# Kernel optimization log

Hardware: AMD Instinct MI355X
Metric: run time of the kernel (lower is better)

## Reference

```python
import jax, jax.numpy as jnp
import numpy as np

IMG = 32            # feature-map side == image_size
B, HC = 8, 3        # batch, hint channels
C, NH, L = 256, 8, 8  # model_channels, nhead, num_encoder_layers
DFF = 1025
HIN = IMG * 8       # hint resolution (three stride-2 convs => /8)
NEIGH = (7, 7)
CONV_SHAPES = [(16, HC), (16, 16), (32, 16), (32, 32), (96, 32), (96, 96), (256, 96), (C, 256)]
STRIDES = [1, 1, 2, 1, 2, 1, 2, 1]


def setup_inputs() -> dict:
    key = jax.random.key(0)
    ks = jax.random.split(key, 32)
    inp = {"hint": jax.random.normal(ks[0], (B, HC, HIN, HIN), jnp.float32)}
    for i, (co, ci) in enumerate(CONV_SHAPES):
        inp[f"conv_w{i}"] = jax.random.normal(ks[1 + i], (co, ci, 3, 3), jnp.float32) * 0.05
    base = 9
    def p(shape, j):
        return jax.random.normal(ks[base + j], (L,) + shape, jnp.float32) * 0.02
    inp["in_proj_w"] = p((3 * C, C), 0)
    inp["in_proj_b"] = p((3 * C,), 1)
    inp["out_w"] = p((C, C), 2)
    inp["out_b"] = p((C,), 3)
    inp["lin1_w"] = p((DFF, C), 4)
    inp["lin1_b"] = p((DFF,), 5)
    inp["lin2_w"] = p((C, DFF), 6)
    inp["lin2_b"] = p((C,), 7)
    inp["ln1_w"] = jnp.ones((L, C), jnp.float32)
    inp["ln1_b"] = jnp.zeros((L, C), jnp.float32)
    inp["ln2_w"] = jnp.ones((L, C), jnp.float32)
    inp["ln2_b"] = jnp.zeros((L, C), jnp.float32)
    return inp


def _conv(x, w, s):
    # torch Conv2d(k=3, padding=1, stride=s, bias=False)
    return jax.lax.conv_general_dilated(x, w, (s, s), [(1, 1), (1, 1)],
                                        dimension_numbers=("NCHW", "OIHW", "NCHW"))


def _sine_pos(h, w, c):
    # DETR/UniAD PositionEmbeddingSine (normalize=False, temperature=1e4) -> (h*w, c)
    npf = c // 2
    y = jnp.broadcast_to(jnp.arange(1, h + 1, dtype=jnp.float32)[:, None], (h, w))
    x = jnp.broadcast_to(jnp.arange(1, w + 1, dtype=jnp.float32)[None, :], (h, w))
    dim_t = 10000.0 ** (2.0 * (jnp.arange(npf, dtype=jnp.float32) // 2) / npf)
    px = x[..., None] / dim_t
    py = y[..., None] / dim_t
    px = jnp.stack([jnp.sin(px[..., 0::2]), jnp.cos(px[..., 1::2])], -1).reshape(h, w, npf)
    py = jnp.stack([jnp.sin(py[..., 0::2]), jnp.cos(py[..., 1::2])], -1).reshape(h, w, npf)
    return jnp.concatenate([py, px], -1).reshape(h * w, c)


def _neigh_mask(h, w, hm, wm):
    # vectorized version of generate_mask: 0 inside the hm x wm neighborhood, -inf outside
    ih = jnp.arange(h)
    iw = jnp.arange(w)
    dh = jnp.abs(ih[:, None] - ih[None, :]) <= hm // 2   # (h, h)
    dw = jnp.abs(iw[:, None] - iw[None, :]) <= wm // 2   # (w, w)
    allowed = (dh[:, None, :, None] & dw[None, :, None, :]).reshape(h * w, h * w)
    return jnp.where(allowed, 0.0, -1e9).astype(jnp.float32)


def _ln(x, g, b):
    mu = x.mean(-1, keepdims=True)
    v = ((x - mu) ** 2).mean(-1, keepdims=True)
    return (x - mu) / jnp.sqrt(v + 1e-5) * g + b


def _forward(hint, conv_ws, params):
    x = hint
    for i, (w, s) in enumerate(zip(conv_ws, STRIDES)):
        x = _conv(x, w, s)
        if i < len(conv_ws) - 1:
            x = jax.nn.silu(x)
    b, c, h, w = x.shape
    src = x.reshape(b, c, h * w).transpose(0, 2, 1)          # (B, N, C), N h-major
    pos = _sine_pos(h, w, c)[None]                           # (1, N, C)
    mask = _neigh_mask(h, w, *NEIGH)                         # (N, N)
    dh = c // NH
    scale = 1.0 / np.sqrt(dh).astype(np.float32)

    def layer(s, p):
        ipw, ipb, ow, ob, l1w, l1b, l2w, l2b, g1, b1, g2, b2 = p
        qk_in = s + pos
        q = (qk_in @ ipw[:c].T + ipb[:c]).reshape(b, -1, NH, dh)
        k = (qk_in @ ipw[c:2 * c].T + ipb[c:2 * c]).reshape(b, -1, NH, dh)
        v = (s @ ipw[2 * c:].T + ipb[2 * c:]).reshape(b, -1, NH, dh)
        sc = jnp.einsum('bnhd,bmhd->bhnm', q, k) * scale + mask
        a = jax.nn.softmax(sc, -1)
        ctx = jnp.einsum('bhnm,bmhd->bnhd', a, v).reshape(b, -1, c)
        s = _ln(s + ctx @ ow.T + ob, g1, b1)                 # post-norm
        ff = jax.nn.relu(s @ l1w.T + l1b) @ l2w.T + l2b      # dropout inactive (eval)
        return _ln(s + ff, g2, b2), None

    src, _ = jax.lax.scan(layer, src, params)
    return src.transpose(0, 2, 1).reshape(b, c, h, w)        # '(h w) b c -> b c h w'


def reference(hint, conv_w0, conv_w1, conv_w2, conv_w3, conv_w4, conv_w5, conv_w6, conv_w7,
              in_proj_w, in_proj_b, out_w, out_b, lin1_w, lin1_b, lin2_w, lin2_b,
              ln1_w, ln1_b, ln2_w, ln2_b):
    conv_ws = (conv_w0, conv_w1, conv_w2, conv_w3, conv_w4, conv_w5, conv_w6, conv_w7)
    params = (in_proj_w, in_proj_b, out_w, out_b, lin1_w, lin1_b, lin2_w, lin2_b,
              ln1_w, ln1_b, ln2_w, ln2_b)
    return _forward(hint, conv_ws, params)
```

## Files before the change

### kernel.cpp

```cpp
#include <hip/hip_runtime.h>
#include <hip/hip_bf16.h>


typedef __bf16 bf16x8 __attribute__((ext_vector_type(8)));
typedef float f32x4 __attribute__((ext_vector_type(4)));
typedef unsigned short us8v __attribute__((ext_vector_type(8)));

__device__ __forceinline__ unsigned short f2bf(float f) {
  unsigned int u = __float_as_uint(f);
  unsigned int r = (u + 0x7fffu + ((u >> 16) & 1u)) >> 16;
  return (unsigned short)r;
}
__device__ __forceinline__ float bf2f(unsigned short h) {
  return __uint_as_float(((unsigned int)h) << 16);
}

#define GLD16(src, dst)                                                        \
  __builtin_amdgcn_global_load_lds(                                            \
      (const __attribute__((address_space(1))) unsigned int*)(src),            \
      (__attribute__((address_space(3))) unsigned int*)(dst), 16, 0, 0)

template<int BM, int BN, int NT, int MODE, int LNF = 0, int KTC = 0>
__global__ __launch_bounds__(NT) void k_gemm(
    const unsigned short* __restrict__ A, int lda,
    const unsigned short* __restrict__ Bw, int ldb,
    const float* __restrict__ bias, const float* __restrict__ posadd,
    float* __restrict__ C, unsigned short* __restrict__ Cb, int ldc,
    int K, int Nstore, int act, int omode, long long zsB, long long zsC,
    const unsigned short* __restrict__ zpage, int Ci, int Hi, int stride, int lw,
    int divm, int divs, const float* __restrict__ lng, const float* __restrict__ lnb)
{
  constexpr int NW = NT / 64;
  constexpr int NWN = (NT == 512) ? 4 : ((BN >= 128) ? 2 : 1);
  constexpr int NWM = NW / NWN;
  constexpr int WM = BM / NWM, WN = BN / NWN;
  constexpr int MF = WM / 16, NF = WN / 16;
  constexpr int AIS = (BM * 8) / NT;
  constexpr int BIS = (BN * 8) / NT;
  __shared__ unsigned short lA[2][BM * 64];
  __shared__ unsigned short lB[2][BN * 64];
  int tid = threadIdx.x, lane = tid & 63, wid = tid >> 6;
  int bm = blockIdx.x * BM, bn = blockIdx.y * BN;
  const unsigned short* Bz = Bw + (size_t)blockIdx.z * zsB;

  int j = (lane & 7) ^ (lane >> 3);
  int e8 = (j & 3) << 3;
  int halfl = j >> 2;

  size_t arow[AIS], brow[BIS];
  int hb[AIS], wb[AIS];
  size_t ab[AIS];
#pragma unroll
  for (int i = 0; i < AIS; ++i) {
    int rr = (wid + i * NW) * 8 + (lane >> 3);
    if constexpr (MODE == 0) {
      arow[i] = (size_t)(bm + rr) * lda + (j << 3);
    } else {
      int pos = bm + rr;
      int b = pos >> (2 * lw);
      int rem = pos & ((1 << (2 * lw)) - 1);
      int ho = rem >> lw, wo = rem & ((1 << lw) - 1);
      hb[i] = ho * stride - 1;
      wb[i] = wo * stride - 1;
      ab[i] = (size_t)b * Hi * Hi * Ci;
    }
  }
#pragma unroll
  for (int i = 0; i < BIS; ++i)
    brow[i] = (size_t)(bn + (wid + i * NW) * 8 + (lane >> 3)) * ldb + (j << 3);

  auto stage = [&](int buf, int kt) {
    if constexpr (MODE == 1) {
      int s0 = kt * 2, s1 = s0 + 1;
      int t0 = (s0 * divm) >> divs, t1 = (s1 * divm) >> divs;
      int cipw = Ci >> 5;
      int cc0 = (s0 - t0 * cipw) << 5, cc1 = (s1 - t1 * cipw) << 5;
      int kh0 = (t0 * 171) >> 9, kw0 = t0 - kh0 * 3;
      int kh1 = (t1 * 171) >> 9, kw1 = t1 - kh1 * 3;
      int kh = halfl ? kh1 : kh0;
      int kw = halfl ? kw1 : kw0;
      int cco = halfl ? cc1 : cc0;
      bool tv = (halfl ? t1 : t0) < 9;
#pragma unroll
      for (int i = 0; i < AIS; ++i) {
        int hi = hb[i] + kh, wi = wb[i] + kw;
        const unsigned short* ap =
            (tv && (unsigned)hi < (unsigned)Hi && (unsigned)wi < (unsigned)Hi)
                ? (A + ab[i] + (size_t)(hi * Hi + wi) * Ci + cco + e8)
                : zpage;
        GLD16(ap, &lA[buf][(wid + i * NW) * 512]);
      }
    } else {
#pragma unroll
      for (int i = 0; i < AIS; ++i)
        GLD16(A + arow[i] + kt * 64, &lA[buf][(wid + i * NW) * 512]);
    }
#pragma unroll
    for (int i = 0; i < BIS; ++i)
      GLD16(Bz + brow[i] + kt * 64, &lB[buf][(wid + i * NW) * 512]);
  };

  f32x4 acc[MF][NF];
#pragma unroll
  for (int m = 0; m < MF; ++m)
#pragma unroll
    for (int n = 0; n < NF; ++n)
#pragma unroll
      for (int q = 0; q < 4; ++q) acc[m][n][q] = 0.f;

  int wn = wid % NWN, wm = wid / NWN;
  int r0 = wm * WM + (lane & 15);
  int c0 = wn * WN + (lane & 15);
  int sl0 = (((lane >> 4)) ^ (lane & 7)) << 3;
  int sl1 = (((lane >> 4) + 4) ^ (lane & 7)) << 3;
  const int nkt = (KTC > 0) ? KTC : (K >> 6);
  int cur = 0;
  stage(0, 0);
#pragma unroll
  for (int kt = 0; kt < nkt; ++kt) {
    if (kt + 1 < nkt) {
      stage(cur ^ 1, kt + 1);
      asm volatile("s_waitcnt vmcnt(%0)" : : "n"(AIS + BIS) : "memory");
    } else {
      asm volatile("s_waitcnt vmcnt(0)" : : : "memory");
    }
    __builtin_amdgcn_s_barrier();
    asm volatile("" ::: "memory");
    bf16x8 a0[MF], a1[MF], b0[NF], b1[NF];
#pragma unroll
    for (int m = 0; m < MF; ++m) {
      a0[m] = *(const bf16x8*)&lA[cur][(r0 + m * 16) * 64 + sl0];
      a1[m] = *(const bf16x8*)&lA[cur][(r0 + m * 16) * 64 + sl1];
    }
#pragma unroll
    for (int n = 0; n < NF; ++n) {
      b0[n] = *(const bf16x8*)&lB[cur][(c0 + n * 16) * 64 + sl0];
      b1[n] = *(const bf16x8*)&lB[cur][(c0 + n * 16) * 64 + sl1];
    }
#pragma unroll
    for (int m = 0; m < MF; ++m)
#pragma unroll
      for (int n = 0; n < NF; ++n)
        acc[m][n] = __builtin_amdgcn_mfma_f32_16x16x32_bf16(a0[m], b0[n], acc[m][n], 0, 0, 0);
#pragma unroll
    for (int m = 0; m < MF; ++m)
#pragma unroll
      for (int n = 0; n < NF; ++n)
        acc[m][n] = __builtin_amdgcn_mfma_f32_16x16x32_bf16(a1[m], b1[n], acc[m][n], 0, 0, 0);
    asm volatile("" ::: "memory");
    __builtin_amdgcn_s_barrier();
    cur ^= 1;
  }

  int colb = bn + wn * WN + (lane & 15);
  int rowb = bm + wm * WM + ((lane >> 4) << 2);
  float* Cz = C ? C + (size_t)blockIdx.z * zsC : nullptr;
  unsigned short* Cbz = Cb ? Cb + (size_t)blockIdx.z * zsC : nullptr;
#pragma unroll
  for (int n = 0; n < NF; ++n) {
    int col = colb + n * 16;
    if (col >= Nstore) continue;
    float bs = bias ? bias[col] : 0.f;
#pragma unroll
    for (int m = 0; m < MF; ++m) {
#pragma unroll
      for (int q = 0; q < 4; ++q) {
        int row = rowb + m * 16 + q;
        float v = acc[m][n][q] + bs;
        if (posadd && col < 512) v += posadd[((row & 1023) << 9) + col];
        if (act == 1) v = fmaxf(v, 0.f);
        else if (act == 2) v = v / (1.f + __expf(-v));
        size_t off = (size_t)row * ldc + col;
        if (omode == 0) Cz[off] = v;
        else if (omode == 1) Cbz[off] = f2bf(v);
        else { Cz[off] = v; Cbz[off] = f2bf(v); }
      }
    }
  }
}

__global__ __launch_bounds__(256) void k_mlp(
    const unsigned short* __restrict__ ctx, const unsigned short* __restrict__ wo,
    const float* __restrict__ ob,
    const unsigned short* __restrict__ w1, const float* __restrict__ b1,
    const unsigned short* __restrict__ w2, const float* __restrict__ b2,
    float* __restrict__ src, unsigned short* __restrict__ sbo,
    const float* __restrict__ g1, const float* __restrict__ lb1,
    const float* __restrict__ g2, const float* __restrict__ lb2)
{
  __shared__ unsigned short aT[4][32 * 64];
  __shared__ unsigned short lB[4][128 * 64];
  __shared__ unsigned short ffl[32][1160];
  __shared__ float red[2][32][2];
  int tid = threadIdx.x, lane = tid & 63, wid = tid >> 6;
  int bm = blockIdx.x << 5;
  int rsrc = lane >> 3;
  int jj8 = ((lane & 7) ^ rsrc) << 3;

  {
    int rr = wid * 8 + rsrc;
    const unsigned short* ap = ctx + (size_t)(bm + rr) * 256 + jj8;
#pragma unroll
    for (int kt = 0; kt < 4; ++kt)
      GLD16(ap + kt * 64, &aT[kt][wid * 512]);
  }

  auto issue = [&](int s) {
    const unsigned short* base;
    int ld, coloff, row0;
    if (s < 8)       { base = wo; ld = 256;  coloff = (s >> 1) * 64; row0 = (s & 1) * 128; }
    else if (s < 44) { int t = s - 8;  base = w1; ld = 256;  coloff = (t & 3) * 64; row0 = (t >> 2) * 128; }
    else             { int t = s - 44; base = w2; ld = 1152; coloff = (t >> 1) * 64; row0 = (t & 1) * 128; }
    int buf = s & 3;
#pragma unroll
    for (int i = 0; i < 4; ++i) {
      int rr = row0 + (wid + i * 4) * 8 + rsrc;
      GLD16(base + (size_t)rr * ld + coloff + jj8, &lB[buf][(wid + i * 4) * 512]);
    }
  };
  issue(0); issue(1); issue(2); issue(3);

  int wn = wid & 1, wm = wid >> 1;
  int r0 = wm * 16 + (lane & 15);
  int sl0 = ((lane >> 4) ^ (lane & 7)) << 3;
  int sl1 = (((lane >> 4) + 4) ^ (lane & 7)) << 3;
  int kqa = (lane >> 4) << 3;
  int cbase = wn * 16 + (lane & 15);
  int rowl = wm * 16 + ((lane >> 4) << 2);

  f32x4 acco[8];
#pragma unroll
  for (int m = 0; m < 8; ++m)
#pragma unroll
    for (int q = 0; q < 4; ++q) acco[m][q] = 0.f;
#pragma unroll
  for (int s = 0; s < 8; ++s) {
    const int kt = s >> 1, rh = s & 1;
    asm volatile("s_waitcnt vmcnt(12)" ::: "memory");
    __builtin_amdgcn_s_barrier();
    asm volatile("" ::: "memory");
    bf16x8 a0 = *(const bf16x8*)&aT[kt][r0 * 64 + sl0];
    bf16x8 a1 = *(const bf16x8*)&aT[kt][r0 * 64 + sl1];
    bf16x8 b0v[4], b1v[4];
#pragma unroll
    for (int nn = 0; nn < 4; ++nn) {
      int rowb = cbase + nn * 32;
      b0v[nn] = *(const bf16x8*)&lB[s & 3][rowb * 64 + sl0];
      b1v[nn] = *(const bf16x8*)&lB[s & 3][rowb * 64 + sl1];
    }
    __builtin_amdgcn_s_setprio(1);
#pragma unroll
    for (int nn = 0; nn < 4; ++nn)
      acco[rh * 4 + nn] = __builtin_amdgcn_mfma_f32_16x16x32_bf16(a0, b0v[nn], acco[rh * 4 + nn], 0, 0, 0);
#pragma unroll
    for (int nn = 0; nn < 4; ++nn)
      acco[rh * 4 + nn] = __builtin_amdgcn_mfma_f32_16x16x32_bf16(a1, b1v[nn], acco[rh * 4 + nn], 0, 0, 0);
    __builtin_amdgcn_s_setprio(0);
    asm volatile("" ::: "memory");
    __builtin_amdgcn_s_barrier();
    issue(s + 4);
  }

  float resid[8][4];
  {
    float x[8][4];
    float sums[4] = {0.f, 0.f, 0.f, 0.f}, sqs[4] = {0.f, 0.f, 0.f, 0.f};
#pragma unroll
    for (int m = 0; m < 8; ++m) {
      int col = ((m >> 2) << 7) + cbase + ((m & 3) << 5);
      float bs = ob[col];
#pragma unroll
      for (int q = 0; q < 4; ++q) {
        float v = acco[m][q] + bs + src[(size_t)(bm + rowl + q) * 256 + col];
        x[m][q] = v;
        sums[q] += v;
        sqs[q] += v * v;
      }
    }
#pragma unroll
    for (int q = 0; q < 4; ++q) {
      sums[q] += __shfl_xor(sums[q], 1); sqs[q] += __shfl_xor(sqs[q], 1);
      sums[q] += __shfl_xor(sums[q], 2); sqs[q] += __shfl_xor(sqs[q], 2);
      sums[q] += __shfl_xor(sums[q], 4); sqs[q] += __shfl_xor(sqs[q], 4);
      sums[q] += __shfl_xor(sums[q], 8); sqs[q] += __shfl_xor(sqs[q], 8);
    }
    if ((lane & 15) == 0) {
#pragma unroll
      for (int q = 0; q < 4; ++q) {
        red[wn][rowl + q][0] = sums[q];
        red[wn][rowl + q][1] = sqs[q];
      }
    }
    asm volatile("s_waitcnt lgkmcnt(0)" ::: "memory");
    __builtin_amdgcn_s_barrier();
    asm volatile("" ::: "memory");
#pragma unroll
    for (int q = 0; q < 4; ++q) {
      float ts = sums[q] + red[wn ^ 1][rowl + q][0];
      float tq = sqs[q] + red[wn ^ 1][rowl + q][1];
      float mu = ts * (1.f / 256.f);
      float var = tq * (1.f / 256.f) - mu * mu;
      float rs = rsqrtf(var + 1e-5f);
      int r = rowl + q;
#pragma unroll
      for (int m = 0; m < 8; ++m) {
        int col = ((m >> 2) << 7) + cbase + ((m & 3) << 5);
        float o = (x[m][q] - mu) * rs * g1[col] + lb1[col];
        resid[m][q] = o;
        int kt = col >> 6, jjc = (col >> 3) & 7, e = col & 7;
        aT[kt][r * 64 + ((jjc ^ (r & 7)) << 3) + e] = f2bf(o);
      }
    }
  }
  asm volatile("s_waitcnt lgkmcnt(0)" ::: "memory");
  __builtin_amdgcn_s_barrier();
  asm volatile("" ::: "memory");

  for (int ny = 0; ny < 9; ++ny) {
    f32x4 acc1[4];
#pragma unroll
    for (int nn = 0; nn < 4; ++nn)
#pragma unroll
      for (int q = 0; q < 4; ++q) acc1[nn][q] = 0.f;
#pragma unroll
    for (int kt = 0; kt < 4; ++kt) {
      int s = 8 + ny * 4 + kt;
      asm volatile("s_waitcnt vmcnt(12)" ::: "memory");
      __builtin_amdgcn_s_barrier();
      asm volatile("" ::: "memory");
      bf16x8 a0 = *(const bf16x8*)&aT[kt][r0 * 64 + sl0];
      bf16x8 a1 = *(const bf16x8*)&aT[kt][r0 * 64 + sl1];
      bf16x8 b0v[4], b1v[4];
#pragma unroll
      for (int nn = 0; nn < 4; ++nn) {
        int rowb = cbase + nn * 32;
        b0v[nn] = *(const bf16x8*)&lB[s & 3][rowb * 64 + sl0];
        b1v[nn] = *(const bf16x8*)&lB[s & 3][rowb * 64 + sl1];
      }
      __builtin_amdgcn_s_setprio(1);
#pragma unroll
      for (int nn = 0; nn < 4; ++nn)
        acc1[nn] = __builtin_amdgcn_mfma_f32_16x16x32_bf16(a0, b0v[nn], acc1[nn], 0, 0, 0);
#pragma unroll
      for (int nn = 0; nn < 4; ++nn)
        acc1[nn] = __builtin_amdgcn_mfma_f32_16x16x32_bf16(a1, b1v[nn], acc1[nn], 0, 0, 0);
      __builtin_amdgcn_s_setprio(0);
      asm volatile("" ::: "memory");
      __builtin_amdgcn_s_barrier();
      issue(s + 4);
    }
#pragma unroll
    for (int nn = 0; nn < 4; ++nn) {
      int col = ny * 128 + cbase + nn * 32;
      float bs = b1[col];
#pragma unroll
      for (int q = 0; q < 4; ++q)
        ffl[rowl + q][col] = f2bf(fmaxf(acc1[nn][q] + bs, 0.f));
    }
  }
  asm volatile("s_waitcnt lgkmcnt(0)" ::: "memory");

  f32x4 acc[8];
#pragma unroll
  for (int m = 0; m < 8; ++m)
#pragma unroll
    for (int q = 0; q < 4; ++q) acc[m][q] = 0.f;
  for (int kt = 0; kt < 18; ++kt) {
#pragma unroll
    for (int rh = 0; rh < 2; ++rh) {
      int t = kt * 2 + rh;
      if (t <= 32) { asm volatile("s_waitcnt vmcnt(12)" ::: "memory"); }
      else if (t == 33) { asm volatile("s_waitcnt vmcnt(8)" ::: "memory"); }
      else if (t == 34) { asm volatile("s_waitcnt vmcnt(4)" ::: "memory"); }
      else { asm volatile("s_waitcnt vmcnt(0)" ::: "memory"); }
      __builtin_amdgcn_s_barrier();
      asm volatile("" ::: "memory");
      bf16x8 a0 = *(const bf16x8*)&ffl[r0][kt * 64 + kqa];
      bf16x8 a1 = *(const bf16x8*)&ffl[r0][kt * 64 + 32 + kqa];
      bf16x8 b0v[4], b1v[4];
#pragma unroll
      for (int nn = 0; nn < 4; ++nn) {
        int rowb = cbase + nn * 32;
        b0v[nn] = *(const bf16x8*)&lB[(44 + t) & 3][rowb * 64 + sl0];
        b1v[nn] = *(const bf16x8*)&lB[(44 + t) & 3][rowb * 64 + sl1];
      }
      __builtin_amdgcn_s_setprio(1);
#pragma unroll
      for (int nn = 0; nn < 4; ++nn)
        acc[rh * 4 + nn] = __builtin_amdgcn_mfma_f32_16x16x32_bf16(a0, b0v[nn], acc[rh * 4 + nn], 0, 0, 0);
#pragma unroll
      for (int nn = 0; nn < 4; ++nn)
        acc[rh * 4 + nn] = __builtin_amdgcn_mfma_f32_16x16x32_bf16(a1, b1v[nn], acc[rh * 4 + nn], 0, 0, 0);
      __builtin_amdgcn_s_setprio(0);
      asm volatile("" ::: "memory");
      __builtin_amdgcn_s_barrier();
      if (t < 32) issue(48 + t);
    }
  }

  float x[8][4];
  float sums[4] = {0.f, 0.f, 0.f, 0.f}, sqs[4] = {0.f, 0.f, 0.f, 0.f};
#pragma unroll
  for (int m = 0; m < 8; ++m) {
    int col = ((m >> 2) << 7) + cbase + ((m & 3) << 5);
    float bs = b2[col];
#pragma unroll
    for (int q = 0; q < 4; ++q) {
      float v = acc[m][q] + bs + resid[m][q];
      x[m][q] = v;
      sums[q] += v;
      sqs[q] += v * v;
    }
  }
#pragma unroll
  for (int q = 0; q < 4; ++q) {
    sums[q] += __shfl_xor(sums[q], 1); sqs[q] += __shfl_xor(sqs[q], 1);
    sums[q] += __shfl_xor(sums[q], 2); sqs[q] += __shfl_xor(sqs[q], 2);
    sums[q] += __shfl_xor(sums[q], 4); sqs[q] += __shfl_xor(sqs[q], 4);
    sums[q] += __shfl_xor(sums[q], 8); sqs[q] += __shfl_xor(sqs[q], 8);
  }
  __syncthreads();
  if ((lane & 15) == 0) {
#pragma unroll
    for (int q = 0; q < 4; ++q) {
      red[wn][rowl + q][0] = sums[q];
      red[wn][rowl + q][1] = sqs[q];
    }
  }
  __syncthreads();
#pragma unroll
  for (int q = 0; q < 4; ++q) {
    float ts = sums[q] + red[wn ^ 1][rowl + q][0];
    float tq = sqs[q] + red[wn ^ 1][rowl + q][1];
    float mu = ts * (1.f / 256.f);
    float var = tq * (1.f / 256.f) - mu * mu;
    float rs = rsqrtf(var + 1e-5f);
    int row = bm + rowl + q;
#pragma unroll
    for (int m = 0; m < 8; ++m) {
      int col = ((m >> 2) << 7) + cbase + ((m & 3) << 5);
      float o = (x[m][q] - mu) * rs * g2[col] + lb2[col];
      src[(size_t)row * 256 + col] = o;
      sbo[(size_t)row * 256 + col] = f2bf(o);
    }
  }
}

__global__ __launch_bounds__(256) void k_conv0(
    const float* __restrict__ x, const float* __restrict__ w,
    unsigned short* __restrict__ y)
{
  __shared__ float ws[16][28];
  int tid = threadIdx.x;
  for (int u = tid; u < 432; u += 256) {
    int co = u / 27, k = u - co * 27;
    int t = k / 3, ci = k - t * 3;
    ws[co][k] = w[((size_t)co * 3 + ci) * 9 + t];
  }
  __syncthreads();
  int h = blockIdx.x, b = blockIdx.y, wo = tid;
  float xin[3][3][3];
#pragma unroll
  for (int ci = 0; ci < 3; ++ci)
#pragma unroll
    for (int kh = 0; kh < 3; ++kh) {
      int hi = h + kh - 1;
#pragma unroll
      for (int kw = 0; kw < 3; ++kw) {
        int wi = wo + kw - 1;
        xin[ci][kh][kw] = ((unsigned)hi < 256u && (unsigned)wi < 256u)
            ? x[(((size_t)b * 3 + ci) << 16) + (hi << 8) + wi] : 0.f;
      }
    }
  float acc[16] = {};
#pragma unroll
  for (int t = 0; t < 9; ++t) {
    const int kh = t / 3, kw = t % 3;
#pragma unroll
    for (int ci = 0; ci < 3; ++ci) {
      float xv = xin[ci][kh][kw];
#pragma unroll
      for (int co = 0; co < 16; ++co)
        acc[co] = fmaf(xv, ws[co][t * 3 + ci], acc[co]);
    }
  }
  us8v o0, o1, zv;
#pragma unroll
  for (int q = 0; q < 8; ++q) {
    float v0 = acc[q];     v0 = v0 / (1.f + __expf(-v0)); o0[q] = f2bf(v0);
    float v1 = acc[q + 8]; v1 = v1 / (1.f + __expf(-v1)); o1[q] = f2bf(v1);
    zv[q] = 0;
  }
  unsigned short* yp = y + ((((size_t)b << 16) + (h << 8) + wo) << 5);
  *(us8v*)(yp) = o0; *(us8v*)(yp + 8) = o1;
  *(us8v*)(yp + 16) = zv; *(us8v*)(yp + 24) = zv;
}

template<int S>
__global__ __launch_bounds__(256) void k_conv_direct(
    const unsigned short* __restrict__ x, const unsigned short* __restrict__ wp,
    int ldw, unsigned short* __restrict__ y, int Hi, int Ho, int Wo, int lwt)
{
  constexpr int HR = 7 * S + 3;
  constexpr int HC = 15 * S + 3;
  constexpr int HP = HR * HC;
  __shared__ unsigned short xs[HP * 40];
  __shared__ unsigned short wsh[32 * 312];
  int tid = threadIdx.x, lane = tid & 63, wv = tid >> 6;
  int b = blockIdx.y;
  int tr = blockIdx.x >> lwt, tc = blockIdx.x & ((1 << lwt) - 1);
  int hi0 = tr * 8 * S - 1, wi0 = tc * 16 * S - 1;

  for (int u = tid; u < HP * 8; u += 256) {
    int pix = u >> 3, part = u & 7;
    int hr = pix / HC, hcc = pix - hr * HC;
    int hi = hi0 + hr, wi = wi0 + hcc;
    ushort4 v = {0, 0, 0, 0};
    if ((unsigned)hi < (unsigned)Hi && (unsigned)wi < (unsigned)Hi)
      v = *(const ushort4*)(x + ((size_t)(b * Hi + hi) * Hi + wi) * 32 + part * 4);
    *(ushort4*)(&xs[pix * 40 + part * 4]) = v;
  }
  for (int u = tid; u < 2304; u += 256) {
    int co = u / 72, kk = (u - co * 72) * 4;
    *(ushort4*)(&wsh[co * 312 + kk]) = *(const ushort4*)(wp + (size_t)co * ldw + kk);
  }
  __syncthreads();

  int cL = lane & 15, kq = (lane >> 4) << 3;
  f32x4 acc[2][2];
#pragma unroll
  for (int m = 0; m < 2; ++m)
#pragma unroll
    for (int n = 0; n < 2; ++n)
#pragma unroll
      for (int q = 0; q < 4; ++q) acc[m][n][q] = 0.f;

#pragma unroll
  for (int tap = 0; tap < 9; ++tap) {
    const int kh = tap / 3, kw = tap % 3;
    bf16x8 af[2], bfr[2];
#pragma unroll
    for (int m = 0; m < 2; ++m) {
      int hr = (wv * 2 + m) * S + kh;
      int hc = cL * S + kw;
      af[m] = *(const bf16x8*)&xs[(hr * HC + hc) * 40 + kq];
    }
#pragma unroll
    for (int n = 0; n < 2; ++n)
      bfr[n] = *(const bf16x8*)&wsh[(cL + n * 16) * 312 + tap * 32 + kq];
#pragma unroll
    for (int m = 0; m < 2; ++m)
#pragma unroll
      for (int n = 0; n < 2; ++n)
        acc[m][n] = __builtin_amdgcn_mfma_f32_16x16x32_bf16(af[m], bfr[n], acc[m][n], 0, 0, 0);
  }

  int wo0 = tc * 16 + ((lane >> 4) << 2);
#pragma unroll
  for (int m = 0; m < 2; ++m) {
    int ho = tr * 8 + wv * 2 + m;
#pragma unroll
    for (int n = 0; n < 2; ++n) {
      int co = cL + n * 16;
#pragma unroll
      for (int q = 0; q < 4; ++q) {
        float v = acc[m][n][q];
        v = v / (1.f + __expf(-v));
        y[((size_t)(b * Ho + ho) * Wo + wo0 + q) * 32 + co] = f2bf(v);
      }
    }
  }
}

struct WP8 { const float* w[8]; unsigned short* q[8]; };
__global__ __launch_bounds__(256) void k_wperm_all(WP8 p)
{
  const int CoPs[8]  = {128, 32, 32, 32, 128, 128, 256, 256};
  const int CiRs[8]  = {3, 16, 16, 32, 32, 96, 96, 256};
  const int CiPs[8]  = {3, 32, 32, 32, 32, 96, 96, 256};
  const int Kpads[8] = {64, 288, 288, 288, 320, 896, 896, 2304};
  const int Cos[8]   = {16, 16, 32, 32, 96, 96, 256, 256};
  int i = blockIdx.y + 1;
  const float* w = p.w[i];
  unsigned short* wp = p.q[i];
  int Kpad = Kpads[i], CiP = CiPs[i], CiR = CiRs[i], Co = Cos[i];
  int total = CoPs[i] * Kpad;
  for (int idx = blockIdx.x * 256 + threadIdx.x; idx < total; idx += gridDim.x * 256) {
    int co = idx / Kpad, k = idx - co * Kpad;
    int t = k / CiP, ci = k - t * CiP;
    float v = 0.f;
    if (co < Co && t < 9 && ci < CiR) v = w[((size_t)co * CiR + ci) * 9 + t];
    wp[idx] = f2bf(v);
  }
}

struct PrepArgs {
  const float *ipw, *outw, *l1w, *l2w, *l1b;
  unsigned short *wqkvb, *outwb, *l1wb, *l2wb, *posb;
  float *l1bp;
};
__global__ __launch_bounds__(256) void k_prep(PrepArgs a)
{
  int seg = blockIdx.y;
  int idx0 = blockIdx.x * 256 + threadIdx.x;
  int stride = gridDim.x * 256;
  if (seg == 0) {
    for (int i = idx0; i < 8 * 768 * 256; i += stride) a.wqkvb[i] = f2bf(a.ipw[i]);
  } else if (seg == 1) {
    for (int i = idx0; i < 8 * 256 * 256; i += stride) a.outwb[i] = f2bf(a.outw[i]);
  } else if (seg == 2) {
    for (int i = idx0; i < 8 * 1152 * 256; i += stride) {
      int l = i / (1152 * 256), r = (i >> 8) % 1152, c = i & 255;
      float v = (r < 1025) ? a.l1w[((size_t)l * 1025 + r) * 256 + c] : 0.f;
      a.l1wb[i] = f2bf(v);
    }
  } else if (seg == 3) {
    for (int i = idx0; i < 8 * 256 * 1152; i += stride) {
      int l = i / (256 * 1152), rc = i % (256 * 1152), r = rc / 1152, c = rc - (rc / 1152) * 1152;
      float v = (c < 1025) ? a.l2w[((size_t)l * 256 + r) * 1025 + c] : 0.f;
      a.l2wb[i] = f2bf(v);
    }
  } else if (seg == 4) {
    for (int i = idx0; i < 8 * 1152; i += stride) {
      int l = i / 1152, c = i - l * 1152;
      a.l1bp[i] = (c < 1025) ? a.l1b[l * 1025 + c] : 0.f;
    }
  } else {
    for (int i = idx0; i < 1024 * 256; i += stride) {
      int n = i >> 8, c = i & 255;
      int ih = n >> 5, iw = n & 31;
      float coord = (c < 128) ? (float)(ih + 1) : (float)(iw + 1);
      int cc = c & 127;
      float e = (float)((cc >> 1) << 1) * (1.f / 128.f);
      float t = coord / powf(10000.f, e);
      a.posb[i] = f2bf((cc & 1) ? cosf(t) : sinf(t));
    }
  }
}

__global__ __launch_bounds__(256) void k_attn(
    const unsigned short* __restrict__ qkv, unsigned short* __restrict__ ctx)
{
  __shared__ unsigned short k_ldsu[848 * 8];
  __shared__ unsigned short v_lds[848 * 8];
  __shared__ float p_lds[64 * 50];
  int bx = blockIdx.x;
  int b = bx >> 4, tile = bx & 15;
  int th8 = ((tile >> 2) << 3), tw8 = ((tile & 3) << 3);
  int g = blockIdx.y;
  int tid = threadIdx.x, lane = tid & 63, wid = tid >> 6;
  int h0e = max(th8 - 3, 0), h1e = min(th8 + 10, 31);
  int w0e = max(tw8 - 3, 0), w1e = min(tw8 + 10, 31);
  int nh = h1e - h0e + 1, nw = w1e - w0e + 1;
  int nkeys = nh * nw, nslots = nkeys * 4;
  unsigned int magic = (65536u + (unsigned)nw - 1u) / (unsigned)nw;
  size_t qbase = (size_t)((unsigned)b << 10) * 768;

#pragma unroll
  for (int i = 0; i < 4; ++i) {
    int base = i * 256 + wid * 64;
    if (base < 784) {
      int s = min(base + lane, nslots - 1);
      int uidx = s >> 2, chunk = s & 3;
      int hh = (int)(((unsigned)uidx * magic) >> 16);
      int ww = uidx - hh * nw;
      hh += h0e; ww += w0e;
      const unsigned short* rp = qkv + qbase + (size_t)((hh << 5) + ww) * 768 + (g << 5) + chunk * 8;
      GLD16(rp + 256, &k_ldsu[base * 8]);
      GLD16(rp + 512, &v_lds[base * 8]);
    }
  }
  __syncthreads();

  int q = tid >> 2, dq = tid & 3;
  int qh = th8 + (q >> 3), qw = tw8 + (q & 7);
  const float scale = 0.17677669529663687f;
  const unsigned short* qp = qkv + qbase + (size_t)((qh << 5) + qw) * 768 + (g << 5) + dq * 8;
  us8v uq = *(const us8v*)qp;
  float qr[8];
#pragma unroll
  for (int t = 0; t < 8; ++t) qr[t] = bf2f(uq[t]) * scale;

  int rbase[7], cofs[7];
  bool rval[7], cval[7];
#pragma unroll
  for (int d = 0; d < 7; ++d) {
    int mh = qh - 3 + d;
    rval[d] = (unsigned)mh < 32u;
    rbase[d] = (mh - h0e) * nw;
    int mw = qw - 3 + d;
    cval[d] = (unsigned)mw < 32u;
    cofs[d] = mw - w0e;
  }

  float m = -1e30f;
#pragma unroll
  for (int kk = 0; kk < 49; ++kk) {
    const int d7 = kk / 7, r7 = kk % 7;
    bool valid = rval[d7] && cval[r7];
    int uidx = valid ? (rbase[d7] + cofs[r7]) : 0;
    us8v uk = *(const us8v*)&k_ldsu[uidx * 32 + dq * 8];
    float d = 0.f;
#pragma unroll
    for (int t = 0; t < 8; ++t) d = fmaf(qr[t], bf2f(uk[t]), d);
    d += __shfl_xor(d, 1);
    d += __shfl_xor(d, 2);
    float s_kk = valid ? d : -1e30f;
    m = fmaxf(m, s_kk);
    if (dq == (kk & 3)) p_lds[q * 50 + kk] = s_kk;
  }
  float sum = 0.f;
  for (int kk = dq; kk < 49; kk += 4) {
    float e = __expf(p_lds[q * 50 + kk] - m);
    p_lds[q * 50 + kk] = e;
    sum += e;
  }
  sum += __shfl_xor(sum, 1);
  sum += __shfl_xor(sum, 2);
  float inv = 1.f / sum;

  float acc[8] = {};
#pragma unroll
  for (int kk = 0; kk < 49; ++kk) {
    const int d7 = kk / 7, r7 = kk % 7;
    int uidx = (rval[d7] && cval[r7]) ? (rbase[d7] + cofs[r7]) : 0;
    float pb = p_lds[q * 50 + kk];
    us8v uv = *(const us8v*)&v_lds[uidx * 32 + dq * 8];
#pragma unroll
    for (int t = 0; t < 8; ++t) acc[t] = fmaf(pb, bf2f(uv[t]), acc[t]);
  }
  unsigned short* op = ctx + ((size_t)((b << 10) + (qh << 5) + qw) << 8) + (g << 5) + dq * 8;
  us8v out;
#pragma unroll
  for (int t = 0; t < 8; ++t) out[t] = f2bf(acc[t] * inv);
  *(us8v*)op = out;
}

__global__ void k_nxc_to_cxn(const float* __restrict__ x, float* __restrict__ y)
{
  __shared__ float t[32][33];
  int b = blockIdx.z;
  int c0 = blockIdx.x * 32, n0 = blockIdx.y * 32;
  int tx = threadIdx.x, ty = threadIdx.y;
  t[ty][tx] = x[((size_t)(b * 1024 + n0 + ty)) * 256 + c0 + tx];
  __syncthreads();
  y[((size_t)(b * 256 + c0 + ty)) * 1024 + n0 + tx] = t[tx][ty];
}

extern "C" void kernel_launch(void* const* d_in, const int* in_sizes, int n_in,
                              void* d_out, int out_size, void* d_ws, size_t ws_size,
                              hipStream_t stream)
{
  const float* hint = (const float*)d_in[0];
  const float* cw[8];
  for (int i = 0; i < 8; ++i) cw[i] = (const float*)d_in[1 + i];
  const float* ipw  = (const float*)d_in[9];
  const float* ipb  = (const float*)d_in[10];
  const float* outw = (const float*)d_in[11];
  const float* outb = (const float*)d_in[12];
  const float* l1w  = (const float*)d_in[13];
  const float* l1b  = (const float*)d_in[14];
  const float* l2w  = (const float*)d_in[15];
  const float* l2b  = (const float*)d_in[16];
  const float* g1   = (const float*)d_in[17];
  const float* b1   = (const float*)d_in[18];
  const float* g2   = (const float*)d_in[19];
  const float* b2   = (const float*)d_in[20];

  float* ws = (float*)d_ws;
  size_t off = 0;
  float* bufA = ws + off; off += 8388608;
  float* bufB = ws + off; off += 8388608;
  float* src  = ws + off; off += 2097152;
  unsigned short* srcb = (unsigned short*)(ws + off); off += 1048576;
  unsigned short* posb = (unsigned short*)(ws + off); off += 131072;
  float* posqk = ws + off; off += 4194304;
  unsigned short* wqkvb = (unsigned short*)(ws + off); off += 786432;
  unsigned short* outwb = (unsigned short*)(ws + off); off += 262144;
  unsigned short* l1wb  = (unsigned short*)(ws + off); off += 1179648;
  unsigned short* l2wb  = (unsigned short*)(ws + off); off += 1179648;
  float* l1bp = ws + off; off += 9216;
  unsigned short* cwp[8];
  const int CoPs[8]  = {128, 32, 32, 32, 128, 128, 256, 256};
  const int Kpads[8] = {64, 288, 288, 288, 320, 896, 896, 2304};
  for (int i = 0; i < 8; ++i) { cwp[i] = (unsigned short*)(ws + off); off += ((size_t)CoPs[i] * Kpads[i] + 1) / 2; }
  unsigned short* zpage = (unsigned short*)(ws + off); off += 64;

  hipMemsetAsync(zpage, 0, 256, stream);

  PrepArgs pa;
  pa.ipw = ipw; pa.outw = outw; pa.l1w = l1w; pa.l2w = l2w; pa.l1b = l1b;
  pa.wqkvb = wqkvb; pa.outwb = outwb; pa.l1wb = l1wb; pa.l2wb = l2wb;
  pa.posb = posb; pa.l1bp = l1bp;
  k_prep<<<dim3(256, 6), 256, 0, stream>>>(pa);
  WP8 wpargs;
  for (int i = 0; i < 8; ++i) { wpargs.w[i] = cw[i]; wpargs.q[i] = cwp[i]; }
  k_wperm_all<<<dim3(64, 7), 256, 0, stream>>>(wpargs);

  unsigned short* bufAu = (unsigned short*)bufA;
  unsigned short* bufBu = (unsigned short*)bufB;

#define GEMM_TAIL nullptr, 0, 0, 0, 0, 0, 0, nullptr, nullptr
  k_conv0<<<dim3(256, 8), 256, 0, stream>>>(hint, cw[0], bufAu);
  k_conv_direct<1><<<dim3(512, 8), 256, 0, stream>>>(bufAu, cwp[1], 288, bufBu, 256, 256, 256, 4);
  k_conv_direct<2><<<dim3(128, 8), 256, 0, stream>>>(bufBu, cwp[2], 288, bufAu, 256, 128, 128, 3);
  k_conv_direct<1><<<dim3(128, 8), 256, 0, stream>>>(bufAu, cwp[3], 288, bufBu, 128, 128, 128, 3);
  k_gemm<128, 128, 512, 1, 0, 5><<<dim3(256, 1), 512, 0, stream>>>(
      bufBu, 0, cwp[4], 320, nullptr, nullptr, nullptr, bufAu, 96, 320, 96, 2, 1,
      0, 0, zpage, 32, 128, 2, 6, 1, 0, nullptr, nullptr);
  k_gemm<128, 128, 512, 1, 0, 14><<<dim3(256, 1), 512, 0, stream>>>(
      bufAu, 0, cwp[5], 896, nullptr, nullptr, nullptr, bufBu, 96, 896, 96, 2, 1,
      0, 0, zpage, 96, 64, 1, 6, 171, 9, nullptr, nullptr);
  k_gemm<64, 128, 512, 1, 0, 14><<<dim3(128, 2), 512, 0, stream>>>(
      bufBu, 0, cwp[6], 896, nullptr, nullptr, nullptr, bufAu, 256, 896, 256, 2, 1,
      0, 0, zpage, 96, 64, 2, 5, 171, 9, nullptr, nullptr);
  k_gemm<64, 128, 512, 1><<<dim3(128, 2), 512, 0, stream>>>(
      bufAu, 0, cwp[7], 2304, nullptr, nullptr, src, srcb, 256, 2304, 256, 0, 2,
      0, 0, zpage, 256, 32, 1, 5, 1, 3, nullptr, nullptr);

  k_gemm<64, 128, 512, 0, 0, 4><<<dim3(16, 4, 8), 512, 0, stream>>>(
      posb, 256, wqkvb, 256, nullptr, nullptr, posqk, nullptr, 512, 256, 512, 0, 0,
      196608LL, 524288LL, GEMM_TAIL);

  unsigned short* qkvb = bufAu;
  unsigned short* ctx  = (unsigned short*)(bufA + 3145728);

  for (int l = 0; l < 8; ++l) {
    const unsigned short* wqkv_l = wqkvb + (size_t)l * 768 * 256;
    const float* ipb_l  = ipb  + (size_t)l * 768;
    const unsigned short* outw_l = outwb + (size_t)l * 256 * 256;
    const float* outb_l = outb + (size_t)l * 256;
    const unsigned short* l1w_l = l1wb + (size_t)l * 1152 * 256;
    const float* l1b_l  = l1bp + (size_t)l * 1152;
    const unsigned short* l2w_l = l2wb + (size_t)l * 256 * 1152;
    const float* l2b_l  = l2b  + (size_t)l * 256;
    const float* posqk_l = posqk + (size_t)l * 524288;
    const float* g1_l = g1 + l * 256; const float* b1_l = b1 + l * 256;
    const float* g2_l = g2 + l * 256; const float* b2_l = b2 + l * 256;

    k_gemm<64, 128, 512, 0, 0, 4><<<dim3(128, 6), 512, 0, stream>>>(
        srcb, 256, wqkv_l, 256, ipb_l, posqk_l, nullptr, qkvb, 768, 256, 768, 0, 1,
        0, 0, GEMM_TAIL);
    k_attn<<<dim3(128, 8), 256, 0, stream>>>(qkvb, ctx);
    k_mlp<<<dim3(256), 256, 0, stream>>>(
        ctx, outw_l, outb_l, l1w_l, l1b_l, l2w_l, l2b_l,
        src, srcb, g1_l, b1_l, g2_l, b2_l);
  }

  k_nxc_to_cxn<<<dim3(8, 32, 8), dim3(32, 32), 0, stream>>>(src, (float*)d_out);
}
```

Measured before the change: 844.1 us.

## Interleave FFN lin1/lin2 per chunk to shrink LDS and pipeline to triple buffering

```diff
diff --git a/kernel.cpp b/kernel.cpp
--- a/kernel.cpp
+++ b/kernel.cpp
@@ -189,8 +189,8 @@
     const float* __restrict__ g2, const float* __restrict__ lb2)
 {
   __shared__ unsigned short aT[4][32 * 64];
-  __shared__ unsigned short lB[4][128 * 64];
-  __shared__ unsigned short ffl[32][1160];
+  __shared__ unsigned short lB[3][128 * 64];
+  __shared__ unsigned short pch[32][136];
   __shared__ float red[2][32][2];
   int tid = threadIdx.x, lane = tid & 63, wid = tid >> 6;
   int bm = blockIdx.x << 5;
@@ -204,21 +204,25 @@
     for (int kt = 0; kt < 4; ++kt)
       GLD16(ap + kt * 64, &aT[kt][wid * 512]);
   }
+  asm volatile("s_waitcnt vmcnt(0)" ::: "memory");
 
   auto issue = [&](int s) {
     const unsigned short* base;
     int ld, coloff, row0;
-    if (s < 8)       { base = wo; ld = 256;  coloff = (s >> 1) * 64; row0 = (s & 1) * 128; }
-    else if (s < 44) { int t = s - 8;  base = w1; ld = 256;  coloff = (t & 3) * 64; row0 = (t >> 2) * 128; }
-    else             { int t = s - 44; base = w2; ld = 1152; coloff = (t >> 1) * 64; row0 = (t & 1) * 128; }
-    int buf = s & 3;
+    if (s < 8)  { base = wo; ld = 256; coloff = (s >> 1) * 64; row0 = (s & 1) * 128; }
+    else {
+      int t = s - 8, ny = t >> 3, u = t & 7;
+      if (u < 4) { base = w1; ld = 256;  row0 = ny * 128; coloff = u * 64; }
+      else { int v = u - 4; base = w2; ld = 1152; row0 = (v & 1) * 128; coloff = ny * 128 + (v >> 1) * 64; }
+    }
+    int buf = s % 3;
 #pragma unroll
     for (int i = 0; i < 4; ++i) {
       int rr = row0 + (wid + i * 4) * 8 + rsrc;
       GLD16(base + (size_t)rr * ld + coloff + jj8, &lB[buf][(wid + i * 4) * 512]);
     }
   };
-  issue(0); issue(1); issue(2); issue(3);
+  issue(0); issue(1);
 
   int wn = wid & 1, wm = wid >> 1;
   int r0 = wm * 16 + (lane & 15);
@@ -228,6 +232,14 @@
   int cbase = wn * 16 + (lane & 15);
   int rowl = wm * 16 + ((lane >> 4) << 2);
 
+  auto stage_top = [&](int s) {
+    if (s == 79) { asm volatile("s_waitcnt vmcnt(0)" ::: "memory"); }
+    else         { asm volatile("s_waitcnt vmcnt(4)" ::: "memory"); }
+    __builtin_amdgcn_s_barrier();
+    asm volatile("" ::: "memory");
+    if (s + 2 < 80) issue(s + 2);
+  };
+
   f32x4 acco[8];
 #pragma unroll
   for (int m = 0; m < 8; ++m)
@@ -236,17 +248,15 @@
 #pragma unroll
   for (int s = 0; s < 8; ++s) {
     const int kt = s >> 1, rh = s & 1;
-    asm volatile("s_waitcnt vmcnt(12)" ::: "memory");
-    __builtin_amdgcn_s_barrier();
-    asm volatile("" ::: "memory");
+    stage_top(s);
     bf16x8 a0 = *(const bf16x8*)&aT[kt][r0 * 64 + sl0];
     bf16x8 a1 = *(const bf16x8*)&aT[kt][r0 * 64 + sl1];
     bf16x8 b0v[4], b1v[4];
 #pragma unroll
     for (int nn = 0; nn < 4; ++nn) {
       int rowb = cbase + nn * 32;
-      b0v[nn] = *(const bf16x8*)&lB[s & 3][rowb * 64 + sl0];
-      b1v[nn] = *(const bf16x8*)&lB[s & 3][rowb * 64 + sl1];
+      b0v[nn] = *(const bf16x8*)&lB[s % 3][rowb * 64 + sl0];
+      b1v[nn] = *(const bf16x8*)&lB[s % 3][rowb * 64 + sl1];
     }
     __builtin_amdgcn_s_setprio(1);
 #pragma unroll
@@ -258,7 +268,6 @@
     __builtin_amdgcn_s_setprio(0);
     asm volatile("" ::: "memory");
     __builtin_amdgcn_s_barrier();
-    issue(s + 4);
   }
 
   float resid[8][4];
@@ -316,6 +325,12 @@
   __builtin_amdgcn_s_barrier();
   asm volatile("" ::: "memory");
 
+  f32x4 acc2[8];
+#pragma unroll
+  for (int m = 0; m < 8; ++m)
+#pragma unroll
+    for (int q = 0; q < 4; ++q) acc2[m][q] = 0.f;
+
   for (int ny = 0; ny < 9; ++ny) {
     f32x4 acc1[4];
 #pragma unroll
@@ -323,19 +338,17 @@
 #pragma unroll
       for (int q = 0; q < 4; ++q) acc1[nn][q] = 0.f;
 #pragma unroll
-    for (int kt = 0; kt < 4; ++kt) {
-      int s = 8 + ny * 4 + kt;
-      asm volatile("s_waitcnt vmcnt(12)" ::: "memory");
-      __builtin_amdgcn_s_barrier();
-      asm volatile("" ::: "memory");
-      bf16x8 a0 = *(const bf16x8*)&aT[kt][r0 * 64 + sl0];
-      bf16x8 a1 = *(const bf16x8*)&aT[kt][r0 * 64 + sl1];
+    for (int u = 0; u < 4; ++u) {
+      int s = 8 + ny * 8 + u;
+      stage_top(s);
+      bf16x8 a0 = *(const bf16x8*)&aT[u][r0 * 64 + sl0];
+      bf16x8 a1 = *(const bf16x8*)&aT[u][r0 * 64 + sl1];
       bf16x8 b0v[4], b1v[4];
 #pragma unroll
       for (int nn = 0; nn < 4; ++nn) {
         int rowb = cbase + nn * 32;
-        b0v[nn] = *(const bf16x8*)&lB[s & 3][rowb * 64 + sl0];
-        b1v[nn] = *(const bf16x8*)&lB[s & 3][rowb * 64 + sl1];
+        b0v[nn] = *(const bf16x8*)&lB[s % 3][rowb * 64 + sl0];
+        b1v[nn] = *(const bf16x8*)&lB[s % 3][rowb * 64 + sl1];
       }
       __builtin_amdgcn_s_setprio(1);
 #pragma unroll
@@ -345,56 +358,44 @@
       for (int nn = 0; nn < 4; ++nn)
         acc1[nn] = __builtin_amdgcn_mfma_f32_16x16x32_bf16(a1, b1v[nn], acc1[nn], 0, 0, 0);
       __builtin_amdgcn_s_setprio(0);
+      if (u == 3) {
+#pragma unroll
+        for (int nn = 0; nn < 4; ++nn) {
+          int colc = cbase + nn * 32;
+          float bs = b1[ny * 128 + colc];
+#pragma unroll
+          for (int q = 0; q < 4; ++q)
+            pch[rowl + q][colc] = f2bf(fmaxf(acc1[nn][q] + bs, 0.f));
+        }
+        asm volatile("s_waitcnt lgkmcnt(0)" ::: "memory");
+      }
       asm volatile("" ::: "memory");
       __builtin_amdgcn_s_barrier();
-      issue(s + 4);
-    }
-#pragma unroll
-    for (int nn = 0; nn < 4; ++nn) {
-      int col = ny * 128 + cbase + nn * 32;
-      float bs = b1[col];
-#pragma unroll
-      for (int q = 0; q < 4; ++q)
-        ffl[rowl + q][col] = f2bf(fmaxf(acc1[nn][q] + bs, 0.f));
-    }
-  }
-  asm volatile("s_waitcnt lgkmcnt(0)" ::: "memory");
-
-  f32x4 acc[8];
-#pragma unroll
-  for (int m = 0; m < 8; ++m)
-#pragma unroll
-    for (int q = 0; q < 4; ++q) acc[m][q] = 0.f;
-  for (int kt = 0; kt < 18; ++kt) {
-#pragma unroll
-    for (int rh = 0; rh < 2; ++rh) {
-      int t = kt * 2 + rh;
-      if (t <= 32) { asm volatile("s_waitcnt vmcnt(12)" ::: "memory"); }
-      else if (t == 33) { asm volatile("s_waitcnt vmcnt(8)" ::: "memory"); }
-      else if (t == 34) { asm volatile("s_waitcnt vmcnt(4)" ::: "memory"); }
-      else { asm volatile("s_waitcnt vmcnt(0)" ::: "memory"); }
-      __builtin_amdgcn_s_barrier();
-      asm volatile("" ::: "memory");
-      bf16x8 a0 = *(const bf16x8*)&ffl[r0][kt * 64 + kqa];
-      bf16x8 a1 = *(const bf16x8*)&ffl[r0][kt * 64 + 32 + kqa];
+    }
+#pragma unroll
+    for (int v = 0; v < 4; ++v) {
+      int s = 8 + ny * 8 + 4 + v;
+      stage_top(s);
+      int koff = (v >> 1) * 64;
+      bf16x8 a0 = *(const bf16x8*)&pch[r0][koff + kqa];
+      bf16x8 a1 = *(const bf16x8*)&pch[r0][koff + 32 + kqa];
       bf16x8 b0v[4], b1v[4];
 #pragma unroll
       for (int nn = 0; nn < 4; ++nn) {
         int rowb = cbase + nn * 32;
-        b0v[nn] = *(const bf16x8*)&lB[(44 + t) & 3][rowb * 64 + sl0];
-        b1v[nn] = *(const bf16x8*)&lB[(44 + t) & 3][rowb * 64 + sl1];
+        b0v[nn] = *(const bf16x8*)&lB[s % 3][rowb * 64 + sl0];
+        b1v[nn] = *(const bf16x8*)&lB[s % 3][rowb * 64 + sl1];
       }
       __builtin_amdgcn_s_setprio(1);
 #pragma unroll
       for (int nn = 0; nn < 4; ++nn)
-        acc[rh * 4 + nn] = __builtin_amdgcn_mfma_f32_16x16x32_bf16(a0, b0v[nn], acc[rh * 4 + nn], 0, 0, 0);
+        acc2[(v & 1) * 4 + nn] = __builtin_amdgcn_mfma_f32_16x16x32_bf16(a0, b0v[nn], acc2[(v & 1) * 4 + nn], 0, 0, 0);
 #pragma unroll
       for (int nn = 0; nn < 4; ++nn)
-        acc[rh * 4 + nn] = __builtin_amdgcn_mfma_f32_16x16x32_bf16(a1, b1v[nn], acc[rh * 4 + nn], 0, 0, 0);
+        acc2[(v & 1) * 4 + nn] = __builtin_amdgcn_mfma_f32_16x16x32_bf16(a1, b1v[nn], acc2[(v & 1) * 4 + nn], 0, 0, 0);
       __builtin_amdgcn_s_setprio(0);
       asm volatile("" ::: "memory");
       __builtin_amdgcn_s_barrier();
-      if (t < 32) issue(48 + t);
     }
   }
 
@@ -406,7 +407,7 @@
     float bs = b2[col];
 #pragma unroll
     for (int q = 0; q < 4; ++q) {
-      float v = acc[m][q] + bs + resid[m][q];
+      float v = acc2[m][q] + bs + resid[m][q];
       x[m][q] = v;
       sums[q] += v;
       sqs[q] += v * v;
```

New measurement: 989.6 us. +17.2%, slower.
